# Performance work log

Measured on AMD Instinct MI355X. Metric: run time of the kernel, lower is better.

## Reference

```python
import jax, jax.numpy as jnp
import numpy as np

H = 2048
Q_RANK = 256
SCALE = float(np.sqrt(Q_RANK))


def setup_inputs() -> dict:
    key = jax.random.key(0)
    k_x, k_s, k_a, k_o, k_b = jax.random.split(key, 5)
    B, L = 4, 4096
    x = jax.random.normal(k_x, (B, L, H), dtype=jnp.float32)
    # nn.Linear(H, q_rank, bias=False): weight [q_rank, H]; y = x @ W.T -> store transposed [H, q_rank]
    Ws = jax.random.normal(k_s, (H, Q_RANK), dtype=jnp.float32) / np.sqrt(H)
    Wa = jax.random.normal(k_a, (H, Q_RANK), dtype=jnp.float32) / np.sqrt(H)
    Wo = jax.random.normal(k_o, (H, H), dtype=jnp.float32) / np.sqrt(H)
    bo = jax.random.normal(k_b, (H,), dtype=jnp.float32) * 0.01
    return {"x": x, "Ws": Ws, "Wa": Wa, "Wo": Wo, "bo": bo}


def reference(x, Ws, Wa, Wo, bo):
    # x: [B, L, H]
    B, L, _ = x.shape
    state = jnp.einsum('blh,hr->blr', x, Ws)   # [B, L, r]
    action = jnp.einsum('blh,hr->blr', x, Wa)  # [B, L, r]
    q_values = jnp.einsum('bir,bjr->bij', state, action) / SCALE  # [B, L, L]
    # causal mask: position i attends to j <= i
    causal = jnp.tril(jnp.ones((L, L), dtype=bool))
    q_values = jnp.where(causal, q_values, -jnp.inf)
    weights = jax.nn.softmax(q_values, axis=-1)  # [B, L, L]
    out = jnp.einsum('bij,bjh->bih', weights, x)  # weights @ x (x acts as V)
    return jnp.einsum('bih,ho->bio', out, Wo.T) + bo  # out_proj: y = out @ Wo_lin.T; Wo stored as [H,H] input-major
```

## Files before the change

### kernel.cpp

```cpp
#include <hip/hip_runtime.h>
#include <hip/hip_bf16.h>
#include <cstdint>
#include <cstddef>
#include <cmath>

typedef __bf16 bf16_t;
typedef __bf16 bf16x8 __attribute__((ext_vector_type(8)));
typedef __bf16 bf16x4v __attribute__((ext_vector_type(4)));
typedef float f32x4 __attribute__((ext_vector_type(4)));

#define B_SZ 4
#define L_SZ 4096
#define H_SZ 2048
#define R_SZ 256
#define EXP_SC 0.090168440f
#define E2_ELEMS 8912896L
#define E2_BYTES 17825792L

#define GLDS16(gaddr, laddr)                                                    \
  __builtin_amdgcn_global_load_lds(                                             \
      (const __attribute__((address_space(1))) void*)(gaddr),                   \
      (__attribute__((address_space(3))) void*)(laddr), 16, 0, 0)

__device__ __forceinline__ f32x4 mfma16(bf16x8 a, bf16x8 b, f32x4 c) {
  return __builtin_amdgcn_mfma_f32_16x16x32_bf16(a, b, c, 0, 0, 0);
}

__device__ __forceinline__ float rsum16(float v) {
  v += __shfl_xor(v, 1, 16);
  v += __shfl_xor(v, 2, 16);
  v += __shfl_xor(v, 4, 16);
  v += __shfl_xor(v, 8, 16);
  return v;
}

__global__ void conv_kernel(const float* __restrict__ x, const float* __restrict__ Ws,
                            const float* __restrict__ Wa, const float* __restrict__ Wo,
                            bf16_t* __restrict__ xb, bf16_t* __restrict__ Wst,
                            bf16_t* __restrict__ Wat, bf16_t* __restrict__ Wob,
                            float* __restrict__ lsum) {
  const int tid = blockIdx.x * blockDim.x + threadIdx.x;
  const int stride = gridDim.x * blockDim.x;
  const int n4 = B_SZ * L_SZ * H_SZ / 4;
  for (int i = tid; i < n4; i += stride) {
    float4 v = reinterpret_cast<const float4*>(x)[i];
    bf16x4v o;
    o[0] = (bf16_t)v.x; o[1] = (bf16_t)v.y; o[2] = (bf16_t)v.z; o[3] = (bf16_t)v.w;
    reinterpret_cast<bf16x4v*>(xb)[i] = o;
  }
  for (int idx = tid; idx < R_SZ * H_SZ; idx += stride) {
    const int rr = idx >> 11;
    const int h  = idx & (H_SZ - 1);
    Wst[idx] = (bf16_t)Ws[h * R_SZ + rr];
    Wat[idx] = (bf16_t)Wa[h * R_SZ + rr];
  }
  for (int idx = tid; idx < H_SZ * H_SZ; idx += stride) {
    Wob[idx] = (bf16_t)Wo[idx];
  }
  for (int idx = tid; idx < B_SZ * L_SZ; idx += stride) lsum[idx] = 0.0f;
}


#define G8_STG(P, REGION, BUFOFF, HALF)                                        \
  GLDS16((P)[0], lds + (REGION) + (BUFOFF) + (HALF)*16384 + ldst0);            \
  GLDS16((P)[1], lds + (REGION) + (BUFOFF) + (HALF)*16384 + ldst1);            \
  (P)[0] += 128; (P)[1] += 128;

#define G8_LDA(MH, BO) {                                                       \
  const char* ap_ = lds + (BO) + (MH)*16384;                                   \
  fa[0][0] = *(const bf16x8*)(ap_ + aOff0);                                    \
  fa[0][1] = *(const bf16x8*)(ap_ + aOff1);                                    \
  fa[1][0] = *(const bf16x8*)(ap_ + 4096 + aOff0);                             \
  fa[1][1] = *(const bf16x8*)(ap_ + 4096 + aOff1);                             \
  fa[2][0] = *(const bf16x8*)(ap_ + 8192 + aOff0);                             \
  fa[2][1] = *(const bf16x8*)(ap_ + 8192 + aOff1);                             \
  fa[3][0] = *(const bf16x8*)(ap_ + 12288 + aOff0);                            \
  fa[3][1] = *(const bf16x8*)(ap_ + 12288 + aOff1); }

#define G8_LDB(NH, BO) {                                                       \
  const char* bp_ = lds + 65536 + (BO) + (NH)*16384;                           \
  fb[NH][0][0] = *(const bf16x8*)(bp_ + bOff0);                                \
  fb[NH][0][1] = *(const bf16x8*)(bp_ + bOff1);                                \
  fb[NH][1][0] = *(const bf16x8*)(bp_ + 8192 + bOff0);                         \
  fb[NH][1][1] = *(const bf16x8*)(bp_ + 8192 + bOff1); }

#define G8_MM1(AM, AN, MF, NH, J)                                              \
  acc[AM][AN] = mfma16(fa[MF][1], fb[NH][J][1],                                \
                 mfma16(fa[MF][0], fb[NH][J][0], acc[AM][AN]))

#define G8_MM(MH, NH)                                                          \
  G8_MM1((MH)*4+0, (NH)*2+0, 0, NH, 0); G8_MM1((MH)*4+0, (NH)*2+1, 0, NH, 1); \
  G8_MM1((MH)*4+1, (NH)*2+0, 1, NH, 0); G8_MM1((MH)*4+1, (NH)*2+1, 1, NH, 1); \
  G8_MM1((MH)*4+2, (NH)*2+0, 2, NH, 0); G8_MM1((MH)*4+2, (NH)*2+1, 2, NH, 1); \
  G8_MM1((MH)*4+3, (NH)*2+0, 3, NH, 0); G8_MM1((MH)*4+3, (NH)*2+1, 3, NH, 1)

#define G8_REGION1(BO, S1A, S1B)                                               \
  G8_LDA(0, BO);                                                               \
  G8_LDB(0, BO);                                                               \
  G8_LDB(1, BO);                                                               \
  S1A; S1B;                                                                    \
  __builtin_amdgcn_s_setprio(1);                                               \
  G8_MM(0, 0);                                                                 \
  G8_MM(0, 1);                                                                 \
  __builtin_amdgcn_s_setprio(0);                                               \
  G8_LDA(1, BO);                                                               \
  asm volatile("s_waitcnt lgkmcnt(8)" ::: "memory");                           \
  __builtin_amdgcn_sched_barrier(0);                                           \
  __builtin_amdgcn_s_barrier();

#define G8_REGION2(S2A, S2B, WAITS)                                            \
  S2A; S2B;                                                                    \
  __builtin_amdgcn_s_setprio(1);                                               \
  G8_MM(1, 0);                                                                 \
  G8_MM(1, 1);                                                                 \
  __builtin_amdgcn_s_setprio(0);                                               \
  asm volatile("s_waitcnt lgkmcnt(0)" ::: "memory");                           \
  WAITS;                                                                       \
  __builtin_amdgcn_sched_barrier(0);                                           \
  __builtin_amdgcn_s_barrier();

__device__ __forceinline__ void gemm8_core(
    const char* Ag, const char* Bg, long aRowB, long bRowB, int NT,
    char* lds, f32x4 (&acc)[8][4])
{
  const int t = threadIdx.x;
  const int l = t & 63;
  const int wid = t >> 6;
  const int wr = wid >> 2;
  const int wc = wid & 3;
  const int l15 = l & 15;
  const int l4 = l >> 4;
  const int swzm = (l15 & 7) << 4;
  const int aOff0 = (wr * 16 + l15) * 128 + ((l4 * 16) ^ swzm);
  const int aOff1 = (wr * 16 + l15) * 128 + ((64 + l4 * 16) ^ swzm);
  const int bOff0 = (wc * 16 + l15) * 128 + ((l4 * 16) ^ swzm);
  const int bOff1 = (wc * 16 + l15) * 128 + ((64 + l4 * 16) ^ swzm);
  const int d0 = t * 16, d1 = t * 16 + 8192;
  const int r0 = d0 >> 7, r1 = d1 >> 7;
  const int s0 = (d0 & 127) ^ ((r0 & 7) << 4);
  const int s1 = (d1 & 127) ^ ((r1 & 7) << 4);
  const char* pA0[2] = { Ag + (long)r0 * aRowB + s0, Ag + (long)r1 * aRowB + s1 };
  const char* pA1[2] = { Ag + (long)(128 + r0) * aRowB + s0, Ag + (long)(128 + r1) * aRowB + s1 };
  const char* pB0[2] = { Bg + (long)r0 * bRowB + s0, Bg + (long)r1 * bRowB + s1 };
  const char* pB1[2] = { Bg + (long)(128 + r0) * bRowB + s0, Bg + (long)(128 + r1) * bRowB + s1 };
  const int ldst0 = wid * 1024, ldst1 = wid * 1024 + 8192;
  bf16x8 fa[4][2], fb[2][2][2];

  G8_STG(pA0, 0, 0, 0);
  G8_STG(pB0, 65536, 0, 0);
  G8_STG(pA1, 0, 0, 1);
  G8_STG(pB1, 65536, 0, 1);
  G8_STG(pA0, 0, 32768, 0);
  G8_STG(pB0, 65536, 32768, 0);
  asm volatile("s_waitcnt vmcnt(4)" ::: "memory");
  __builtin_amdgcn_sched_barrier(0);
  __builtin_amdgcn_s_barrier();

  int bufOff = 0;
  for (int T = 0; T < NT - 2; ++T) {
    const int ob = bufOff ^ 32768;
    G8_REGION1(bufOff, G8_STG(pA1, 0, ob, 1), G8_STG(pB1, 65536, ob, 1));
    G8_REGION2(G8_STG(pA0, 0, bufOff, 0), G8_STG(pB0, 65536, bufOff, 0),
               asm volatile("s_waitcnt vmcnt(4)" ::: "memory"));
    bufOff ^= 32768;
  }
  {
    const int ob = bufOff ^ 32768;
    G8_REGION1(bufOff, G8_STG(pA1, 0, ob, 1), G8_STG(pB1, 65536, ob, 1));
    G8_REGION2(, , asm volatile("s_waitcnt vmcnt(0)" ::: "memory"));
    bufOff ^= 32768;
  }
  {
    G8_REGION1(bufOff, , );
    G8_REGION2(, , );
  }
}

__global__ __launch_bounds__(512) void vq8_kernel(
    const bf16_t* __restrict__ Wob, const bf16_t* __restrict__ xb, bf16_t* __restrict__ VT,
    const bf16_t* __restrict__ Wst, const bf16_t* __restrict__ Wat,
    bf16_t* __restrict__ Qb, bf16_t* __restrict__ Kb)
{
  extern __shared__ char lds[];
  const int f = blockIdx.x;
  const int t = threadIdx.x, l = t & 63, wid = t >> 6;
  const int wr = wid >> 2, wc = wid & 3, l15 = l & 15, l4 = l >> 4;
  if (f < 128) {
    const int proj = f >> 6;
    const long mBase = (long)(f & 63) * 256;
    const bf16_t* W = proj ? Wat : Wst;
    bf16_t* Cp = proj ? Kb : Qb;
    f32x4 acc[8][4] = {};
    gemm8_core((const char*)xb + mBase * (H_SZ * 2), (const char*)W,
               H_SZ * 2, H_SZ * 2, H_SZ / 64, lds, acc);
#pragma unroll
    for (int am = 0; am < 8; ++am) {
#pragma unroll
      for (int an = 0; an < 4; ++an) {
        const long row = mBase + wr * 16 + am * 32 + l4 * 4;
        const int col = wc * 16 + an * 64 + l15;
#pragma unroll
        for (int r = 0; r < 4; ++r)
          Cp[(row + r) * R_SZ + col] = (bf16_t)acc[am][an][r];
      }
    }
  } else {
    const int g = f - 128;
    const int lg = (g & 7) * 64 + (g >> 3);
    const int xo = lg & 7;
    const int yj = (lg >> 3) & 15;
    const int b  = lg >> 7;
    const long mBase = (long)xo * 256;
    const long nBase = (long)yj * 256;
    f32x4 acc[8][4] = {};
    gemm8_core((const char*)Wob + mBase * (H_SZ * 2),
               (const char*)xb + ((long)b * L_SZ + nBase) * (H_SZ * 2),
               H_SZ * 2, H_SZ * 2, H_SZ / 64, lds, acc);
    bf16_t* Cp = VT + (long)b * H_SZ * L_SZ;
#pragma unroll
    for (int am = 0; am < 8; ++am) {
#pragma unroll
      for (int an = 0; an < 4; ++an) {
        const long row = mBase + wr * 16 + am * 32 + l4 * 4;
        const long col = nBase + wc * 16 + an * 64 + l15;
#pragma unroll
        for (int r = 0; r < 4; ++r)
          Cp[(row + r) * L_SZ + col] = (bf16_t)acc[am][an][r];
      }
    }
  }
}

__global__ __launch_bounds__(512) void ep8_kernel(
    const bf16_t* __restrict__ Qb, const bf16_t* __restrict__ Kb,
    bf16_t* __restrict__ E, float* __restrict__ lsum)
{
  extern __shared__ char lds[];
  const int f = blockIdx.x;
  const int lg = (f & 7) * 68 + (f >> 3);
  const int b = lg / 136;
  const int t136 = lg - b * 136;
  int P = (int)((sqrtf((float)(8 * t136 + 1)) - 1.0f) * 0.5f);
  while ((P + 1) * (P + 2) / 2 <= t136) ++P;
  while (P * (P + 1) / 2 > t136) --P;
  const int Jp = t136 - P * (P + 1) / 2;

  f32x4 acc[8][4] = {};
  gemm8_core((const char*)Qb + ((long)b * L_SZ + P * 256) * (R_SZ * 2),
             (const char*)Kb + ((long)b * L_SZ + Jp * 256) * (R_SZ * 2),
             R_SZ * 2, R_SZ * 2, R_SZ / 64, lds, acc);
  const int t = threadIdx.x, l = t & 63, wid = t >> 6;
  const int wr = wid >> 2, wc = wid & 3, l15 = l & 15, l4 = l >> 4;
  bf16_t* Ep = E + (long)b * E2_ELEMS + 32768L * P * (P + 1);
  const long ldaE = (long)(P + 1) * 256;
  float* lp = lsum + (long)b * L_SZ + P * 256;
  const bool diag = (Jp == P);
#pragma unroll
  for (int am = 0; am < 8; ++am) {
    const int rowi = wr * 16 + am * 32 + l4 * 4;
#pragma unroll
    for (int r = 0; r < 4; ++r) {
      float s = 0.0f;
#pragma unroll
      for (int an = 0; an < 4; ++an) {
        const int coli = wc * 16 + an * 64 + l15;
        float p = exp2f(acc[am][an][r] * EXP_SC);
        if (diag && coli > rowi + r) p = 0.0f;
        Ep[(long)(rowi + r) * ldaE + Jp * 256 + coli] = (bf16_t)p;
        s += p;
      }
      s = rsum16(s);
      if (l15 == 0) atomicAdd(lp + rowi + r, s);
    }
  }
}

__global__ __launch_bounds__(512) void pv8_kernel(
    const bf16_t* __restrict__ E, const bf16_t* __restrict__ VT,
    const float* __restrict__ lsum, const float* __restrict__ bo,
    float* __restrict__ out)
{
  extern __shared__ char lds[];
  const int f = blockIdx.x;
  const int lg = (f & 7) * 32 + (f >> 3);
  const int yj = lg & 7;
  const int pr = (lg >> 3) & 7;
  const int b  = lg >> 6;
  const int nBase = yj * 256;
  const int t = threadIdx.x, l = t & 63, wid = t >> 6;
  const int wr = wid >> 2, wc = wid & 3, l15 = l & 15, l4 = l >> 4;

#pragma unroll
  for (int s = 0; s < 2; ++s) {
    const int mt = s ? pr : (15 - pr);
    f32x4 acc[8][4] = {};
    const char* Ag = (const char*)E + (long)b * E2_BYTES + 65536L * mt * (mt + 1);
    const char* Bg = (const char*)VT + ((long)b * H_SZ + nBase) * (L_SZ * 2);
    gemm8_core(Ag, Bg, (long)(mt + 1) * 512, L_SZ * 2, (mt + 1) * 4, lds, acc);
#pragma unroll
    for (int am = 0; am < 8; ++am) {
      const long rowG = (long)b * L_SZ + mt * 256 + wr * 16 + am * 32 + l4 * 4;
      float linv[4];
#pragma unroll
      for (int r = 0; r < 4; ++r) linv[r] = 1.0f / lsum[rowG + r];
#pragma unroll
      for (int an = 0; an < 4; ++an) {
        const int col = nBase + wc * 16 + an * 64 + l15;
        const float bias = bo[col];
#pragma unroll
        for (int r = 0; r < 4; ++r)
          out[(rowG + r) * H_SZ + col] = acc[am][an][r] * linv[r] + bias;
      }
    }
  }
}

extern "C" void kernel_launch(void* const* d_in, const int* in_sizes, int n_in,
                              void* d_out, int out_size, void* d_ws, size_t ws_size,
                              hipStream_t stream) {
  const float* x  = (const float*)d_in[0];
  const float* Ws = (const float*)d_in[1];
  const float* Wa = (const float*)d_in[2];
  const float* Wo = (const float*)d_in[3];
  const float* bo = (const float*)d_in[4];
  float* out = (float*)d_out;

  char* ws = (char*)d_ws;
  bf16_t* xb  = (bf16_t*)(ws + 0);
  bf16_t* Wst = (bf16_t*)(ws + 67108864);
  bf16_t* Wat = (bf16_t*)(ws + 68157440);
  bf16_t* Wob = (bf16_t*)(ws + 69206016);
  bf16_t* Qb  = (bf16_t*)(ws + 77594624);
  bf16_t* Kb  = (bf16_t*)(ws + 85983232);
  bf16_t* VT  = (bf16_t*)(ws + 94371840);
  float*  lsum = (float*)(ws + 161480704);
  bf16_t* E   = (bf16_t*)(ws + 0);

  hipFuncSetAttribute((const void*)vq8_kernel, hipFuncAttributeMaxDynamicSharedMemorySize, 131072);
  hipFuncSetAttribute((const void*)ep8_kernel, hipFuncAttributeMaxDynamicSharedMemorySize, 131072);
  hipFuncSetAttribute((const void*)pv8_kernel, hipFuncAttributeMaxDynamicSharedMemorySize, 131072);

  conv_kernel<<<dim3(2048), dim3(256), 0, stream>>>(x, Ws, Wa, Wo, xb, Wst, Wat, Wob, lsum);
  vq8_kernel<<<dim3(640), dim3(512), 131072, stream>>>(Wob, xb, VT, Wst, Wat, Qb, Kb);
  ep8_kernel<<<dim3(544), dim3(512), 131072, stream>>>(Qb, Kb, E, lsum);
  pv8_kernel<<<dim3(256), dim3(512), 131072, stream>>>(E, VT, lsum, bo, out);
}
```

Measured before the change: 374.3 us.

## Switch GEMM core from 16x16x32 to 32x32x16 bf16 MFMA tiles

Replaces the 16x16x32 MFMA inner kernel with the 32x32x16 variant across the shared GEMM core. LDS fragment loads, swizzle offsets and the epilogues of all three GEMM kernels are remapped to the 32x32 output layout. The larger instruction does more work per LDS fragment load and needs fewer instructions, which is meant to raise MFMA throughput. In exchange it changes the LDS access pattern, so bank conflicts may differ. The PV epilogue now divides by lsum once per element instead of reusing a precomputed reciprocal.

```diff
diff --git a/kernel.cpp b/kernel.cpp
--- a/kernel.cpp
+++ b/kernel.cpp
@@ -7,7 +7,7 @@
 typedef __bf16 bf16_t;
 typedef __bf16 bf16x8 __attribute__((ext_vector_type(8)));
 typedef __bf16 bf16x4v __attribute__((ext_vector_type(4)));
-typedef float f32x4 __attribute__((ext_vector_type(4)));
+typedef float f32x16 __attribute__((ext_vector_type(16)));
 
 #define B_SZ 4
 #define L_SZ 4096
@@ -22,15 +22,16 @@
       (const __attribute__((address_space(1))) void*)(gaddr),                   \
       (__attribute__((address_space(3))) void*)(laddr), 16, 0, 0)
 
-__device__ __forceinline__ f32x4 mfma16(bf16x8 a, bf16x8 b, f32x4 c) {
-  return __builtin_amdgcn_mfma_f32_16x16x32_bf16(a, b, c, 0, 0, 0);
-}
-
-__device__ __forceinline__ float rsum16(float v) {
-  v += __shfl_xor(v, 1, 16);
-  v += __shfl_xor(v, 2, 16);
-  v += __shfl_xor(v, 4, 16);
-  v += __shfl_xor(v, 8, 16);
+__device__ __forceinline__ f32x16 mfma32(bf16x8 a, bf16x8 b, f32x16 c) {
+  return __builtin_amdgcn_mfma_f32_32x32x16_bf16(a, b, c, 0, 0, 0);
+}
+
+__device__ __forceinline__ float rsum32(float v) {
+  v += __shfl_xor(v, 1, 32);
+  v += __shfl_xor(v, 2, 32);
+  v += __shfl_xor(v, 4, 32);
+  v += __shfl_xor(v, 8, 32);
+  v += __shfl_xor(v, 16, 32);
   return v;
 }
 
@@ -66,44 +67,44 @@
   GLDS16((P)[1], lds + (REGION) + (BUFOFF) + (HALF)*16384 + ldst1);            \
   (P)[0] += 128; (P)[1] += 128;
 
-#define G8_LDA(MH, BO) {                                                       \
-  const char* ap_ = lds + (BO) + (MH)*16384;                                   \
-  fa[0][0] = *(const bf16x8*)(ap_ + aOff0);                                    \
-  fa[0][1] = *(const bf16x8*)(ap_ + aOff1);                                    \
-  fa[1][0] = *(const bf16x8*)(ap_ + 4096 + aOff0);                             \
-  fa[1][1] = *(const bf16x8*)(ap_ + 4096 + aOff1);                             \
-  fa[2][0] = *(const bf16x8*)(ap_ + 8192 + aOff0);                             \
-  fa[2][1] = *(const bf16x8*)(ap_ + 8192 + aOff1);                             \
-  fa[3][0] = *(const bf16x8*)(ap_ + 12288 + aOff0);                            \
-  fa[3][1] = *(const bf16x8*)(ap_ + 12288 + aOff1); }
-
-#define G8_LDB(NH, BO) {                                                       \
-  const char* bp_ = lds + 65536 + (BO) + (NH)*16384;                           \
-  fb[NH][0][0] = *(const bf16x8*)(bp_ + bOff0);                                \
-  fb[NH][0][1] = *(const bf16x8*)(bp_ + bOff1);                                \
-  fb[NH][1][0] = *(const bf16x8*)(bp_ + 8192 + bOff0);                         \
-  fb[NH][1][1] = *(const bf16x8*)(bp_ + 8192 + bOff1); }
-
-#define G8_MM1(AM, AN, MF, NH, J)                                              \
-  acc[AM][AN] = mfma16(fa[MF][1], fb[NH][J][1],                                \
-                 mfma16(fa[MF][0], fb[NH][J][0], acc[AM][AN]))
-
-#define G8_MM(MH, NH)                                                          \
-  G8_MM1((MH)*4+0, (NH)*2+0, 0, NH, 0); G8_MM1((MH)*4+0, (NH)*2+1, 0, NH, 1); \
-  G8_MM1((MH)*4+1, (NH)*2+0, 1, NH, 0); G8_MM1((MH)*4+1, (NH)*2+1, 1, NH, 1); \
-  G8_MM1((MH)*4+2, (NH)*2+0, 2, NH, 0); G8_MM1((MH)*4+2, (NH)*2+1, 2, NH, 1); \
-  G8_MM1((MH)*4+3, (NH)*2+0, 3, NH, 0); G8_MM1((MH)*4+3, (NH)*2+1, 3, NH, 1)
+#define G32_LDA(MH, BO) {                                                      \
+  const char* ap_ = lds + (BO) + (MH)*16384 + aRowOff;                         \
+  fa[0][0] = *(const bf16x8*)(ap_ + kb0);                                      \
+  fa[0][1] = *(const bf16x8*)(ap_ + kb1);                                      \
+  fa[0][2] = *(const bf16x8*)(ap_ + kb2);                                      \
+  fa[0][3] = *(const bf16x8*)(ap_ + kb3);                                      \
+  fa[1][0] = *(const bf16x8*)(ap_ + 8192 + kb0);                               \
+  fa[1][1] = *(const bf16x8*)(ap_ + 8192 + kb1);                               \
+  fa[1][2] = *(const bf16x8*)(ap_ + 8192 + kb2);                               \
+  fa[1][3] = *(const bf16x8*)(ap_ + 8192 + kb3); }
+
+#define G32_LDB(NH, BO) {                                                      \
+  const char* bp_ = lds + 65536 + (BO) + (NH)*16384 + bRowOff;                 \
+  fb[NH][0] = *(const bf16x8*)(bp_ + kb0);                                     \
+  fb[NH][1] = *(const bf16x8*)(bp_ + kb1);                                     \
+  fb[NH][2] = *(const bf16x8*)(bp_ + kb2);                                     \
+  fb[NH][3] = *(const bf16x8*)(bp_ + kb3); }
+
+#define G32_MM(MH, NH)                                                         \
+  acc[(MH)*2+0][NH] = mfma32(fa[0][0], fb[NH][0], acc[(MH)*2+0][NH]);          \
+  acc[(MH)*2+1][NH] = mfma32(fa[1][0], fb[NH][0], acc[(MH)*2+1][NH]);          \
+  acc[(MH)*2+0][NH] = mfma32(fa[0][1], fb[NH][1], acc[(MH)*2+0][NH]);          \
+  acc[(MH)*2+1][NH] = mfma32(fa[1][1], fb[NH][1], acc[(MH)*2+1][NH]);          \
+  acc[(MH)*2+0][NH] = mfma32(fa[0][2], fb[NH][2], acc[(MH)*2+0][NH]);          \
+  acc[(MH)*2+1][NH] = mfma32(fa[1][2], fb[NH][2], acc[(MH)*2+1][NH]);          \
+  acc[(MH)*2+0][NH] = mfma32(fa[0][3], fb[NH][3], acc[(MH)*2+0][NH]);          \
+  acc[(MH)*2+1][NH] = mfma32(fa[1][3], fb[NH][3], acc[(MH)*2+1][NH])
 
 #define G8_REGION1(BO, S1A, S1B)                                               \
-  G8_LDA(0, BO);                                                               \
-  G8_LDB(0, BO);                                                               \
-  G8_LDB(1, BO);                                                               \
+  G32_LDA(0, BO);                                                              \
+  G32_LDB(0, BO);                                                              \
+  G32_LDB(1, BO);                                                              \
   S1A; S1B;                                                                    \
   __builtin_amdgcn_s_setprio(1);                                               \
-  G8_MM(0, 0);                                                                 \
-  G8_MM(0, 1);                                                                 \
+  G32_MM(0, 0);                                                                \
+  G32_MM(0, 1);                                                                \
   __builtin_amdgcn_s_setprio(0);                                               \
-  G8_LDA(1, BO);                                                               \
+  G32_LDA(1, BO);                                                              \
   asm volatile("s_waitcnt lgkmcnt(8)" ::: "memory");                           \
   __builtin_amdgcn_sched_barrier(0);                                           \
   __builtin_amdgcn_s_barrier();
@@ -111,8 +112,8 @@
 #define G8_REGION2(S2A, S2B, WAITS)                                            \
   S2A; S2B;                                                                    \
   __builtin_amdgcn_s_setprio(1);                                               \
-  G8_MM(1, 0);                                                                 \
-  G8_MM(1, 1);                                                                 \
+  G32_MM(1, 0);                                                                \
+  G32_MM(1, 1);                                                                \
   __builtin_amdgcn_s_setprio(0);                                               \
   asm volatile("s_waitcnt lgkmcnt(0)" ::: "memory");                           \
   WAITS;                                                                       \
@@ -121,20 +122,22 @@
 
 __device__ __forceinline__ void gemm8_core(
     const char* Ag, const char* Bg, long aRowB, long bRowB, int NT,
-    char* lds, f32x4 (&acc)[8][4])
+    char* lds, f32x16 (&acc)[4][2])
 {
   const int t = threadIdx.x;
   const int l = t & 63;
   const int wid = t >> 6;
   const int wr = wid >> 2;
   const int wc = wid & 3;
-  const int l15 = l & 15;
-  const int l4 = l >> 4;
-  const int swzm = (l15 & 7) << 4;
-  const int aOff0 = (wr * 16 + l15) * 128 + ((l4 * 16) ^ swzm);
-  const int aOff1 = (wr * 16 + l15) * 128 + ((64 + l4 * 16) ^ swzm);
-  const int bOff0 = (wc * 16 + l15) * 128 + ((l4 * 16) ^ swzm);
-  const int bOff1 = (wc * 16 + l15) * 128 + ((64 + l4 * 16) ^ swzm);
+  const int l31 = l & 31;
+  const int l5 = l >> 5;
+  const int swz = (l & 7) << 4;
+  const int kb0 = (0 * 32 + l5 * 16) ^ swz;
+  const int kb1 = (1 * 32 + l5 * 16) ^ swz;
+  const int kb2 = (2 * 32 + l5 * 16) ^ swz;
+  const int kb3 = (3 * 32 + l5 * 16) ^ swz;
+  const int aRowOff = (wr * 32 + l31) * 128;
+  const int bRowOff = (wc * 32 + l31) * 128;
   const int d0 = t * 16, d1 = t * 16 + 8192;
   const int r0 = d0 >> 7, r1 = d1 >> 7;
   const int s0 = (d0 & 127) ^ ((r0 & 7) << 4);
@@ -144,7 +147,7 @@
   const char* pB0[2] = { Bg + (long)r0 * bRowB + s0, Bg + (long)r1 * bRowB + s1 };
   const char* pB1[2] = { Bg + (long)(128 + r0) * bRowB + s0, Bg + (long)(128 + r1) * bRowB + s1 };
   const int ldst0 = wid * 1024, ldst1 = wid * 1024 + 8192;
-  bf16x8 fa[4][2], fb[2][2][2];
+  bf16x8 fa[2][4], fb[2][4];
 
   G8_STG(pA0, 0, 0, 0);
   G8_STG(pB0, 65536, 0, 0);
@@ -176,6 +179,10 @@
   }
 }
 
+__device__ __forceinline__ int rb32(int am, int wr) {
+  return ((am >> 1) * 4 + (am & 1) * 2 + wr) * 32;
+}
+
 __global__ __launch_bounds__(512) void vq8_kernel(
     const bf16_t* __restrict__ Wob, const bf16_t* __restrict__ xb, bf16_t* __restrict__ VT,
     const bf16_t* __restrict__ Wst, const bf16_t* __restrict__ Wat,
@@ -184,48 +191,45 @@
   extern __shared__ char lds[];
   const int f = blockIdx.x;
   const int t = threadIdx.x, l = t & 63, wid = t >> 6;
-  const int wr = wid >> 2, wc = wid & 3, l15 = l & 15, l4 = l >> 4;
+  const int wr = wid >> 2, wc = wid & 3, l31 = l & 31, l5 = l >> 5;
+  long mBase, nBase;
+  const char* Ag;
+  const char* Bg;
+  bf16_t* Cp;
+  long ldc;
   if (f < 128) {
     const int proj = f >> 6;
-    const long mBase = (long)(f & 63) * 256;
-    const bf16_t* W = proj ? Wat : Wst;
-    bf16_t* Cp = proj ? Kb : Qb;
-    f32x4 acc[8][4] = {};
-    gemm8_core((const char*)xb + mBase * (H_SZ * 2), (const char*)W,
-               H_SZ * 2, H_SZ * 2, H_SZ / 64, lds, acc);
-#pragma unroll
-    for (int am = 0; am < 8; ++am) {
-#pragma unroll
-      for (int an = 0; an < 4; ++an) {
-        const long row = mBase + wr * 16 + am * 32 + l4 * 4;
-        const int col = wc * 16 + an * 64 + l15;
-#pragma unroll
-        for (int r = 0; r < 4; ++r)
-          Cp[(row + r) * R_SZ + col] = (bf16_t)acc[am][an][r];
-      }
-    }
+    mBase = (long)(f & 63) * 256;
+    nBase = 0;
+    Ag = (const char*)xb + mBase * (H_SZ * 2);
+    Bg = (const char*)(proj ? Wat : Wst);
+    Cp = proj ? Kb : Qb;
+    ldc = R_SZ;
   } else {
     const int g = f - 128;
     const int lg = (g & 7) * 64 + (g >> 3);
     const int xo = lg & 7;
     const int yj = (lg >> 3) & 15;
     const int b  = lg >> 7;
-    const long mBase = (long)xo * 256;
-    const long nBase = (long)yj * 256;
-    f32x4 acc[8][4] = {};
-    gemm8_core((const char*)Wob + mBase * (H_SZ * 2),
-               (const char*)xb + ((long)b * L_SZ + nBase) * (H_SZ * 2),
-               H_SZ * 2, H_SZ * 2, H_SZ / 64, lds, acc);
-    bf16_t* Cp = VT + (long)b * H_SZ * L_SZ;
-#pragma unroll
-    for (int am = 0; am < 8; ++am) {
-#pragma unroll
-      for (int an = 0; an < 4; ++an) {
-        const long row = mBase + wr * 16 + am * 32 + l4 * 4;
-        const long col = nBase + wc * 16 + an * 64 + l15;
-#pragma unroll
-        for (int r = 0; r < 4; ++r)
-          Cp[(row + r) * L_SZ + col] = (bf16_t)acc[am][an][r];
+    mBase = (long)xo * 256;
+    nBase = (long)yj * 256;
+    Ag = (const char*)Wob + mBase * (H_SZ * 2);
+    Bg = (const char*)xb + ((long)b * L_SZ + nBase) * (H_SZ * 2);
+    Cp = VT + (long)b * H_SZ * L_SZ;
+    ldc = L_SZ;
+  }
+  f32x16 acc[4][2] = {};
+  gemm8_core(Ag, Bg, H_SZ * 2, H_SZ * 2, H_SZ / 64, lds, acc);
+#pragma unroll
+  for (int am = 0; am < 4; ++am) {
+    const int rbase = rb32(am, wr);
+#pragma unroll
+    for (int an = 0; an < 2; ++an) {
+      const long col = nBase + an * 128 + wc * 32 + l31;
+#pragma unroll
+      for (int q = 0; q < 16; ++q) {
+        const long row = mBase + rbase + (q & 3) + 8 * (q >> 2) + 4 * l5;
+        Cp[row * ldc + col] = (bf16_t)acc[am][an][q];
       }
     }
   }
@@ -245,32 +249,33 @@
   while (P * (P + 1) / 2 > t136) --P;
   const int Jp = t136 - P * (P + 1) / 2;
 
-  f32x4 acc[8][4] = {};
+  f32x16 acc[4][2] = {};
   gemm8_core((const char*)Qb + ((long)b * L_SZ + P * 256) * (R_SZ * 2),
              (const char*)Kb + ((long)b * L_SZ + Jp * 256) * (R_SZ * 2),
              R_SZ * 2, R_SZ * 2, R_SZ / 64, lds, acc);
   const int t = threadIdx.x, l = t & 63, wid = t >> 6;
-  const int wr = wid >> 2, wc = wid & 3, l15 = l & 15, l4 = l >> 4;
+  const int wr = wid >> 2, wc = wid & 3, l31 = l & 31, l5 = l >> 5;
   bf16_t* Ep = E + (long)b * E2_ELEMS + 32768L * P * (P + 1);
   const long ldaE = (long)(P + 1) * 256;
   float* lp = lsum + (long)b * L_SZ + P * 256;
   const bool diag = (Jp == P);
 #pragma unroll
-  for (int am = 0; am < 8; ++am) {
-    const int rowi = wr * 16 + am * 32 + l4 * 4;
-#pragma unroll
-    for (int r = 0; r < 4; ++r) {
+  for (int am = 0; am < 4; ++am) {
+    const int rbase = rb32(am, wr);
+#pragma unroll
+    for (int q = 0; q < 16; ++q) {
+      const int rowi = rbase + (q & 3) + 8 * (q >> 2) + 4 * l5;
       float s = 0.0f;
 #pragma unroll
-      for (int an = 0; an < 4; ++an) {
-        const int coli = wc * 16 + an * 64 + l15;
-        float p = exp2f(acc[am][an][r] * EXP_SC);
-        if (diag && coli > rowi + r) p = 0.0f;
-        Ep[(long)(rowi + r) * ldaE + Jp * 256 + coli] = (bf16_t)p;
+      for (int an = 0; an < 2; ++an) {
+        const int coli = an * 128 + wc * 32 + l31;
+        float p = exp2f(acc[am][an][q] * EXP_SC);
+        if (diag && coli > rowi) p = 0.0f;
+        Ep[(long)rowi * ldaE + Jp * 256 + coli] = (bf16_t)p;
         s += p;
       }
-      s = rsum16(s);
-      if (l15 == 0) atomicAdd(lp + rowi + r, s);
+      s = rsum32(s);
+      if (l31 == 0) atomicAdd(lp + rowi, s);
     }
   }
 }
@@ -288,28 +293,27 @@
   const int b  = lg >> 6;
   const int nBase = yj * 256;
   const int t = threadIdx.x, l = t & 63, wid = t >> 6;
-  const int wr = wid >> 2, wc = wid & 3, l15 = l & 15, l4 = l >> 4;
+  const int wr = wid >> 2, wc = wid & 3, l31 = l & 31, l5 = l >> 5;
 
 #pragma unroll
   for (int s = 0; s < 2; ++s) {
     const int mt = s ? pr : (15 - pr);
-    f32x4 acc[8][4] = {};
+    f32x16 acc[4][2] = {};
     const char* Ag = (const char*)E + (long)b * E2_BYTES + 65536L * mt * (mt + 1);
     const char* Bg = (const char*)VT + ((long)b * H_SZ + nBase) * (L_SZ * 2);
     gemm8_core(Ag, Bg, (long)(mt + 1) * 512, L_SZ * 2, (mt + 1) * 4, lds, acc);
 #pragma unroll
-    for (int am = 0; am < 8; ++am) {
-      const long rowG = (long)b * L_SZ + mt * 256 + wr * 16 + am * 32 + l4 * 4;
-      float linv[4];
-#pragma unroll
-      for (int r = 0; r < 4; ++r) linv[r] = 1.0f / lsum[rowG + r];
-#pragma unroll
-      for (int an = 0; an < 4; ++an) {
-        const int col = nBase + wc * 16 + an * 64 + l15;
-        const float bias = bo[col];
-#pragma unroll
-        for (int r = 0; r < 4; ++r)
-          out[(rowG + r) * H_SZ + col] = acc[am][an][r] * linv[r] + bias;
+    for (int am = 0; am < 4; ++am) {
+      const int rbase = rb32(am, wr);
+#pragma unroll
+      for (int an = 0; an < 2; ++an) {
+        const int colG = nBase + an * 128 + wc * 32 + l31;
+        const float bias = bo[colG];
+#pragma unroll
+        for (int q = 0; q < 16; ++q) {
+          const long rowG = (long)b * L_SZ + mt * 256 + rbase + (q & 3) + 8 * (q >> 2) + 4 * l5;
+          out[rowG * H_SZ + colG] = acc[am][an][q] / lsum[rowG] + bias;
+        }
       }
     }
   }
```

Measured after the change: 493.2 us. +31.8%, slower.
